# Performance work log

Hardware: AMD Instinct MI355X
Metric: run time of the kernel (lower is better)

The kernel has to match this reference:

```python
import jax, jax.numpy as jnp
import numpy as np

B, S, H, L = 4, 1024, 1024, 4
NH, NKV, HD = 16, 8, 64
F, V, W = 3072, 32000, 12
THETA = 1000000.0
EPS = 1e-6
NEG = -1e9


def _rms(x, w):
    return (x * jax.lax.rsqrt(jnp.mean(jnp.square(x), axis=-1, keepdims=True) + EPS)) * w


def _rotate_half(x):
    x1, x2 = jnp.split(x, 2, axis=-1)
    return jnp.concatenate([-x2, x1], axis=-1)


def setup_inputs() -> dict:
    key = jax.random.key(0)
    ks = jax.random.split(key, 16)
    s = 0.02
    return {
        'input_ids': jax.random.randint(ks[0], (B, S), 0, V),
        'attention_mask': jnp.ones((B, S), dtype=jnp.int32),
        'embed': jax.random.normal(ks[1], (V, H), jnp.float32) * s,
        'wq': jax.random.normal(ks[2], (L, H, NH * HD), jnp.float32) * s,
        'wk': jax.random.normal(ks[3], (L, H, NKV * HD), jnp.float32) * s,
        'wv': jax.random.normal(ks[4], (L, H, NKV * HD), jnp.float32) * s,
        'wo': jax.random.normal(ks[5], (L, NH * HD, H), jnp.float32) * s,
        'q_norm_w': jnp.ones((L, HD), jnp.float32),
        'k_norm_w': jnp.ones((L, HD), jnp.float32),
        'ln1': jnp.ones((L, H), jnp.float32),
        'ln2': jnp.ones((L, H), jnp.float32),
        'w_gate': jax.random.normal(ks[6], (L, H, F), jnp.float32) * s,
        'w_up': jax.random.normal(ks[7], (L, H, F), jnp.float32) * s,
        'w_down': jax.random.normal(ks[8], (L, F, H), jnp.float32) * s,
        'final_norm': jnp.ones((H,), jnp.float32),
    }


def _forward(embed, wq, wk, wv, wo, q_norm_w, k_norm_w, ln1, ln2,
             w_gate, w_up, w_down, final_norm, input_ids, attention_mask):
    h = embed[input_ids]                                   # [B,S,H]
    # rotary embeddings (Qwen3 style, theta=1e6)
    pos = jnp.arange(S, dtype=jnp.float32)
    inv_freq = 1.0 / (THETA ** (jnp.arange(0, HD, 2, dtype=jnp.float32) / HD))
    freqs = pos[:, None] * inv_freq[None, :]               # [S, HD/2]
    emb = jnp.concatenate([freqs, freqs], axis=-1)         # [S, HD]
    cos = jnp.cos(emb)[None, :, None, :]
    sin = jnp.sin(emb)[None, :, None, :]
    # masks: full = expanded (non-causal) padding mask; sliding = +/-W band
    pad = (1.0 - attention_mask.astype(jnp.float32))[:, None, None, :] * NEG
    idx = jnp.arange(S)
    band = jnp.abs(idx[:, None] - idx[None, :]) <= W       # [S,S]
    full_mask = jnp.broadcast_to(pad, (B, 1, S, S))
    slide_mask = jnp.where(band[None, None], full_mask, NEG)
    scale = 1.0 / np.sqrt(HD).astype(np.float32)
    for l in range(L):
        mask = full_mask if l % 2 == 0 else slide_mask     # attention_type dispatch
        x = _rms(h, ln1[l])
        q = _rms((x @ wq[l]).reshape(B, S, NH, HD), q_norm_w[l])
        k = _rms((x @ wk[l]).reshape(B, S, NKV, HD), k_norm_w[l])
        v = (x @ wv[l]).reshape(B, S, NKV, HD)
        q = q * cos + _rotate_half(q) * sin
        k = k * cos + _rotate_half(k) * sin
        rep = NH // NKV                                    # GQA expand
        k = jnp.repeat(k, rep, axis=2)
        v = jnp.repeat(v, rep, axis=2)
        scores = jnp.einsum('bqhd,bkhd->bhqk', q, k) * scale + mask
        p = jax.nn.softmax(scores, axis=-1)
        attn = jnp.einsum('bhqk,bkhd->bqhd', p, v).reshape(B, S, NH * HD)
        h = h + attn @ wo[l]
        x = _rms(h, ln2[l])
        h = h + (jax.nn.silu(x @ w_gate[l]) * (x @ w_up[l])) @ w_down[l]
    return _rms(h, final_norm)


def reference(input_ids, attention_mask, embed, wq, wk, wv, wo, q_norm_w, k_norm_w,
              ln1, ln2, w_gate, w_up, w_down, final_norm):
    return _forward(embed, wq, wk, wv, wo, q_norm_w, k_norm_w, ln1, ln2,
                    w_gate, w_up, w_down, final_norm, input_ids, attention_mask)
```

## Files before the change

kernel.cpp:

```cpp
#include <hip/hip_runtime.h>
#include <math.h>

#define BB 4
#define SS 1024
#define HH 1024
#define LL 4
#define NHH 16
#define NKV 8
#define HD 64
#define FF 3072
#define WW 12
#define NEG_INF (-1e9f)

#define OQ  0
#define OK_ 1048576
#define OV  1572864
#define OO  2097152
#define OG  3145728
#define OU  6291456
#define OD  9437184

typedef __attribute__((ext_vector_type(8))) short bf16x8;
typedef __attribute__((ext_vector_type(4))) float f32x4;
typedef __attribute__((ext_vector_type(16))) float f32x16;
typedef __attribute__((ext_vector_type(8))) unsigned short u16x8;

__device__ __forceinline__ unsigned short f2bf(float f) {
    union { float f; unsigned int u; } v; v.f = f;
    unsigned int r = (v.u + 0x7fffu + ((v.u >> 16) & 1u)) >> 16;
    return (unsigned short)r;
}
__device__ __forceinline__ float bf2f(unsigned short u) {
    union { unsigned int u; float f; } v; v.u = ((unsigned int)u) << 16;
    return v.f;
}
__device__ __forceinline__ unsigned int pkbf(float lo, float hi) {
    return (unsigned int)f2bf(lo) | ((unsigned int)f2bf(hi) << 16);
}
__device__ __forceinline__ void gll16(const void* g, void* l) {
    __builtin_amdgcn_global_load_lds((const __attribute__((address_space(1))) void*)g,
                                     (__attribute__((address_space(3))) void*)l, 16, 0, 0);
}

__global__ __launch_bounds__(256) void k_embed(const int* __restrict__ ids,
                                               const float* __restrict__ embed,
                                               float* __restrict__ h) {
    int row = blockIdx.x, tid = threadIdx.x;
    int id = ids[row];
    ((float4*)(h + (size_t)row * HH))[tid] = ((const float4*)(embed + (size_t)id * HH))[tid];
}

__global__ __launch_bounds__(256) void k_rms_bf16(const float* __restrict__ in,
                                                  const float* __restrict__ w,
                                                  unsigned short* __restrict__ out) {
    __shared__ float red[4];
    int row = blockIdx.x, tid = threadIdx.x;
    float4 v = ((const float4*)(in + (size_t)row * HH))[tid];
    float ss = v.x * v.x + v.y * v.y + v.z * v.z + v.w * v.w;
#pragma unroll
    for (int off = 1; off < 64; off <<= 1) ss += __shfl_xor(ss, off);
    if ((tid & 63) == 0) red[tid >> 6] = ss;
    __syncthreads();
    float tot = red[0] + red[1] + red[2] + red[3];
    float scale = rsqrtf(tot * (1.0f / HH) + 1e-6f);
    float4 wv = ((const float4*)w)[tid];
    ushort4 o;
    o.x = f2bf(v.x * scale * wv.x); o.y = f2bf(v.y * scale * wv.y);
    o.z = f2bf(v.z * scale * wv.z); o.w = f2bf(v.w * scale * wv.w);
    *(ushort4*)&out[(size_t)row * HH + tid * 4] = o;
}

template <int NP, int BF16OUT>
__global__ __launch_bounds__(256) void k_rms_add(float* __restrict__ h,
                                                 const float* __restrict__ p0,
                                                 const float* __restrict__ p1,
                                                 const float* __restrict__ p2,
                                                 const float* __restrict__ w,
                                                 void* __restrict__ outx) {
    __shared__ float red[4];
    int row = blockIdx.x, tid = threadIdx.x;
    size_t base = (size_t)row * HH;
    float4 v = ((const float4*)(h + base))[tid];
    float4 a = ((const float4*)(p0 + base))[tid];
    v.x += a.x; v.y += a.y; v.z += a.z; v.w += a.w;
    if (NP > 1) {
        float4 b = ((const float4*)(p1 + base))[tid];
        v.x += b.x; v.y += b.y; v.z += b.z; v.w += b.w;
    }
    if (NP > 2) {
        float4 c = ((const float4*)(p2 + base))[tid];
        v.x += c.x; v.y += c.y; v.z += c.z; v.w += c.w;
    }
    ((float4*)(h + base))[tid] = v;
    float ss = v.x * v.x + v.y * v.y + v.z * v.z + v.w * v.w;
#pragma unroll
    for (int off = 1; off < 64; off <<= 1) ss += __shfl_xor(ss, off);
    if ((tid & 63) == 0) red[tid >> 6] = ss;
    __syncthreads();
    float tot = red[0] + red[1] + red[2] + red[3];
    float scale = rsqrtf(tot * (1.0f / HH) + 1e-6f);
    float4 wv = ((const float4*)w)[tid];
    float rx = v.x * scale * wv.x, ry = v.y * scale * wv.y;
    float rz = v.z * scale * wv.z, rw = v.w * scale * wv.w;
    if (BF16OUT) {
        ushort4 o;
        o.x = f2bf(rx); o.y = f2bf(ry); o.z = f2bf(rz); o.w = f2bf(rw);
        *(ushort4*)&((unsigned short*)outx)[base + tid * 4] = o;
    } else {
        float4 o; o.x = rx; o.y = ry; o.z = rz; o.w = rw;
        ((float4*)((float*)outx + base))[tid] = o;
    }
}

__global__ __launch_bounds__(256) void k_cast_all(const float* __restrict__ wq,
                                                  const float* __restrict__ wk,
                                                  const float* __restrict__ wv,
                                                  const float* __restrict__ wo,
                                                  const float* __restrict__ wg,
                                                  const float* __restrict__ wu,
                                                  const float* __restrict__ wd,
                                                  unsigned short* __restrict__ wbf) {
    __shared__ float t[64][65];
    int tI = blockIdx.x;
    const float* W; unsigned short* Wt; int N, K, local;
    if (tI < 256)       { W = wq; Wt = wbf + OQ;  N = 1024; K = 1024; local = tI; }
    else if (tI < 384)  { W = wk; Wt = wbf + OK_; N = 512;  K = 1024; local = tI - 256; }
    else if (tI < 512)  { W = wv; Wt = wbf + OV;  N = 512;  K = 1024; local = tI - 384; }
    else if (tI < 768)  { W = wo; Wt = wbf + OO;  N = 1024; K = 1024; local = tI - 512; }
    else if (tI < 1536) { W = wg; Wt = wbf + OG;  N = 3072; K = 1024; local = tI - 768; }
    else if (tI < 2304) { W = wu; Wt = wbf + OU;  N = 3072; K = 1024; local = tI - 1536; }
    else                { W = wd; Wt = wbf + OD;  N = 1024; K = 3072; local = tI - 2304; }
    int tn = N >> 6;
    int n0 = (local % tn) * 64, k0 = (local / tn) * 64;
    int tid = threadIdx.x;
    int r = tid >> 4;
    int c4 = (tid & 15) * 4;
#pragma unroll
    for (int e = 0; e < 4; ++e) {
        int kk = r + e * 16;
        float4 vv = *(const float4*)&W[(size_t)(k0 + kk) * N + n0 + c4];
        t[c4 + 0][kk] = vv.x;
        t[c4 + 1][kk] = vv.y;
        t[c4 + 2][kk] = vv.z;
        t[c4 + 3][kk] = vv.w;
    }
    __syncthreads();
#pragma unroll
    for (int e = 0; e < 4; ++e) {
        int nn = r + e * 16;
        ushort4 o;
        o.x = f2bf(t[nn][c4 + 0]);
        o.y = f2bf(t[nn][c4 + 1]);
        o.z = f2bf(t[nn][c4 + 2]);
        o.w = f2bf(t[nn][c4 + 3]);
        *(ushort4*)&Wt[(size_t)(n0 + nn) * K + k0 + c4] = o;
    }
}

template <int EPI>
__device__ __forceinline__ void mgemm_core(const unsigned short* __restrict__ A,
                                           const unsigned short* __restrict__ Bt,
                                           void* __restrict__ Cv,
                                           int N, int K, int lda, int ldb,
                                           int bm, int bn) {
    __shared__ unsigned short As[128 * 32];
    __shared__ unsigned short Bs[128 * 32];
    int tid = threadIdx.x;
    int w = tid >> 6, l = tid & 63;
    int wr = (w >> 1) * 64, wc = (w & 1) * 64;

    f32x4 acc[4][4] = {};

    for (int k0 = 0; k0 < K; k0 += 32) {
        __syncthreads();
#pragma unroll
        for (int i = 0; i < 2; ++i) {
            int cb = i * 256 + w * 64;
            int c = cb + l;
            const unsigned short* ga = A + (size_t)(bm + (c >> 2)) * lda + k0 + (c & 3) * 8;
            const unsigned short* gb = Bt + (size_t)(bn + (c >> 2)) * ldb + k0 + (c & 3) * 8;
            gll16(ga, As + cb * 8);
            gll16(gb, Bs + cb * 8);
        }
        __syncthreads();

        bf16x8 af[4], bfr[4];
#pragma unroll
        for (int i = 0; i < 4; ++i) {
            int m = wr + i * 16 + (l & 15);
            af[i] = *(const bf16x8*)&As[m * 32 + (l >> 4) * 8];
            int n = wc + i * 16 + (l & 15);
            bfr[i] = *(const bf16x8*)&Bs[n * 32 + (l >> 4) * 8];
        }
#pragma unroll
        for (int i = 0; i < 4; ++i)
#pragma unroll
            for (int j = 0; j < 4; ++j)
                acc[i][j] = __builtin_amdgcn_mfma_f32_16x16x32_bf16(af[i], bfr[j], acc[i][j], 0, 0, 0);
    }

#pragma unroll
    for (int i = 0; i < 4; ++i) {
        int rbase = bm + wr + i * 16 + (l >> 4) * 4;
#pragma unroll
        for (int j = 0; j < 4; ++j) {
            int col = bn + wc + j * 16 + (l & 15);
#pragma unroll
            for (int r = 0; r < 4; ++r) {
                size_t off = (size_t)(rbase + r) * N + col;
                if (EPI == 0) ((float*)Cv)[off] = acc[i][j][r];
                else if (EPI == 1) ((float*)Cv)[off] += acc[i][j][r];
                else ((unsigned short*)Cv)[off] = f2bf(acc[i][j][r]);
            }
        }
    }
}

template <int PARTS>
__global__ __launch_bounds__(256) void k_mgemm_splitk(const unsigned short* __restrict__ A,
                                                      const unsigned short* __restrict__ Bt,
                                                      float* __restrict__ p0,
                                                      float* __restrict__ p1,
                                                      float* __restrict__ p2,
                                                      int N, int Ktot) {
    int part = blockIdx.z;
    int Kp = Ktot / PARTS;
    float* C = (part == 0) ? p0 : (part == 1 ? p1 : p2);
    mgemm_core<0>(A + part * Kp, Bt + part * Kp, C, N, Kp, Ktot, Ktot,
                  blockIdx.y * 128, blockIdx.x * 128);
}

__global__ __launch_bounds__(256) void k_mgemm_qkv(const unsigned short* __restrict__ A,
                                                   const unsigned short* __restrict__ wqt,
                                                   const unsigned short* __restrict__ wkt,
                                                   const unsigned short* __restrict__ wvt,
                                                   float* __restrict__ q,
                                                   float* __restrict__ k,
                                                   unsigned short* __restrict__ v) {
    int nt = blockIdx.x;
    if (nt < 8)       mgemm_core<0>(A, wqt, q, 1024, 1024, 1024, 1024, blockIdx.y * 128, nt * 128);
    else if (nt < 12) mgemm_core<0>(A, wkt, k, 512, 1024, 1024, 1024, blockIdx.y * 128, (nt - 8) * 128);
    else              mgemm_core<2>(A, wvt, v, 512, 1024, 1024, 1024, blockIdx.y * 128, (nt - 12) * 128);
}

__global__ __launch_bounds__(256) void k_mgemm_gu(const unsigned short* __restrict__ A,
                                                  const unsigned short* __restrict__ wgt,
                                                  const unsigned short* __restrict__ wut,
                                                  unsigned short* __restrict__ g,
                                                  unsigned short* __restrict__ u) {
    int nt = blockIdx.x;
    const unsigned short* Bt = (nt < 24) ? wgt : wut;
    unsigned short* C = (nt < 24) ? g : u;
    int bn = (nt < 24 ? nt : nt - 24) * 128;
    mgemm_core<2>(A, Bt, C, 3072, 1024, 1024, 1024, blockIdx.y * 128, bn);
}

__global__ __launch_bounds__(256) void k_qknorm_rope(const float* __restrict__ qk,
                                                     unsigned short* __restrict__ out,
                                                     const float* __restrict__ nw,
                                                     int nheads) {
    int tid = threadIdx.x;
    int w = tid >> 6, lane = tid & 63;
    int gid = blockIdx.x * 4 + w;
    int row = gid / nheads;
    int pos = row & (SS - 1);
    size_t base = (size_t)gid * HD;
    float xv = qk[base + lane];
    float ss = xv * xv;
#pragma unroll
    for (int off = 1; off < 64; off <<= 1) ss += __shfl_xor(ss, off);
    float scale = rsqrtf(ss * (1.0f / HD) + 1e-6f);
    float xn = xv * scale * nw[lane];
    int j = lane & 31;
    float inv_freq = powf(1.0e6f, -(float)j * (1.0f / 32.0f));
    float f = (float)pos * inv_freq;
    float c = cosf(f), s = sinf(f);
    float partner = __shfl_xor(xn, 32);
    float rot = (lane < 32) ? -partner : partner;
    out[base + lane] = f2bf(xn * c + rot * s);
}

__global__ __launch_bounds__(256) void k_mattn(const unsigned short* __restrict__ q,
                                               const unsigned short* __restrict__ k,
                                               const unsigned short* __restrict__ v,
                                               const int* __restrict__ amask,
                                               unsigned short* __restrict__ out,
                                               int sliding) {
    __shared__ __align__(16) char smem[18432];
    unsigned short* Klds = (unsigned short*)smem;
    unsigned int*   VtU  = (unsigned int*)(smem + 8192);
    float* mlds          = (float*)(smem + 17152);
    unsigned short* Olds = (unsigned short*)smem;

    const int b = blockIdx.z, head = blockIdx.y, q0 = blockIdx.x * 128;
    const int kvh = head >> 1;
    const int tid = threadIdx.x, w = tid >> 6, lane = tid & 63;
    const int h = lane >> 5, ln31 = lane & 31;
    const int qg = q0 + w * 32 + ln31;
    const float sscale = 0.125f;

    bf16x8 qf[4];
    const unsigned short* qrow = q + (size_t)(b * SS + qg) * 1024 + head * 64;
#pragma unroll
    for (int c = 0; c < 4; ++c) qf[c] = *(const bf16x8*)(qrow + c * 16 + h * 8);

    f32x16 O0 = {}, O1 = {};
    float m = -3.4e38f, l_sum = 0.0f;

    int t_lo = 0, t_hi = (SS >> 6) - 1;
    if (sliding) {
        int lo = q0 - WW; if (lo < 0) lo = 0;
        int hi = q0 + 127 + WW; if (hi > SS - 1) hi = SS - 1;
        t_lo = lo >> 6; t_hi = hi >> 6;
    }

    const int vd = tid & 63, vw = tid >> 6;

    for (int t = t_lo; t <= t_hi; ++t) {
        int kv0 = t << 6;
        __syncthreads();
        if (tid < 64) mlds[tid] = amask[b * SS + kv0 + tid] ? 0.0f : NEG_INF;
#pragma unroll
        for (int i = 0; i < 2; ++i) {
            int slot = i * 256 + w * 64 + lane;
            int row = slot >> 3, u = slot & 7;
            int ug = u ^ (row & 7);
            const unsigned short* src = k + (size_t)(b * SS + kv0 + row) * 512 + kvh * 64 + ug * 8;
            gll16(src, Klds + (size_t)slot * 8);
        }
        {
            const unsigned short* vsrc = v + (size_t)(b * SS + kv0 + vw * 16) * 512 + kvh * 64 + vd;
            unsigned short tmp[16];
#pragma unroll
            for (int kk = 0; kk < 16; ++kk) tmp[kk] = vsrc[(size_t)kk * 512];
#pragma unroll
            for (int j = 0; j < 8; ++j)
                VtU[vd * 35 + vw * 8 + j] =
                    (unsigned int)tmp[2 * j] | ((unsigned int)tmp[2 * j + 1] << 16);
        }
        __syncthreads();

        f32x16 a0 = {}, a1 = {};
#pragma unroll
        for (int c = 0; c < 4; ++c) {
            int u = (2 * c + h) ^ (ln31 & 7);
            bf16x8 k0 = *(const bf16x8*)&Klds[ln31 * 64 + u * 8];
            bf16x8 k1 = *(const bf16x8*)&Klds[(32 + ln31) * 64 + u * 8];
            a0 = __builtin_amdgcn_mfma_f32_32x32x16_bf16(k0, qf[c], a0, 0, 0, 0);
            a1 = __builtin_amdgcn_mfma_f32_32x32x16_bf16(k1, qf[c], a1, 0, 0, 0);
        }

        float tmax = -3.4e38f;
#pragma unroll
        for (int r = 0; r < 16; ++r) {
            int kl = (r & 3) + 8 * (r >> 2) + 4 * h;
            float mv0 = mlds[kl], mv1 = mlds[32 + kl];
            if (sliding) {
                int d0 = qg - (kv0 + kl); if (d0 < 0) d0 = -d0;
                int d1 = qg - (kv0 + 32 + kl); if (d1 < 0) d1 = -d1;
                if (d0 > WW) mv0 = NEG_INF;
                if (d1 > WW) mv1 = NEG_INF;
            }
            a0[r] = a0[r] * sscale + mv0;
            a1[r] = a1[r] * sscale + mv1;
            tmax = fmaxf(tmax, fmaxf(a0[r], a1[r]));
        }
        tmax = fmaxf(tmax, __shfl_xor(tmax, 32));
        float nm = fmaxf(m, tmax);
        float corr = __expf(m - nm);
        float tsum = 0.0f;
#pragma unroll
        for (int r = 0; r < 16; ++r) {
            a0[r] = __expf(a0[r] - nm);
            a1[r] = __expf(a1[r] - nm);
            tsum += a0[r] + a1[r];
        }
        tsum += __shfl_xor(tsum, 32);
        l_sum = l_sum * corr + tsum;
#pragma unroll
        for (int r = 0; r < 16; ++r) { O0[r] *= corr; O1[r] *= corr; }
        m = nm;

#pragma unroll
        for (int s = 0; s < 2; ++s) {
#pragma unroll
            for (int c2 = 0; c2 < 2; ++c2) {
                float p0v = s ? a1[8 * c2 + 0] : a0[8 * c2 + 0];
                float p1v = s ? a1[8 * c2 + 1] : a0[8 * c2 + 1];
                float p2v = s ? a1[8 * c2 + 2] : a0[8 * c2 + 2];
                float p3v = s ? a1[8 * c2 + 3] : a0[8 * c2 + 3];
                float p4v = s ? a1[8 * c2 + 4] : a0[8 * c2 + 4];
                float p5v = s ? a1[8 * c2 + 5] : a0[8 * c2 + 5];
                float p6v = s ? a1[8 * c2 + 6] : a0[8 * c2 + 6];
                float p7v = s ? a1[8 * c2 + 7] : a0[8 * c2 + 7];
                unsigned int A0 = pkbf(p0v, p1v);
                unsigned int A1 = pkbf(p2v, p3v);
                unsigned int A2 = pkbf(p4v, p5v);
                unsigned int A3 = pkbf(p6v, p7v);
                unsigned int pA0 = (unsigned int)__shfl_xor((int)A0, 32);
                unsigned int pA1 = (unsigned int)__shfl_xor((int)A1, 32);
                unsigned int pA2 = (unsigned int)__shfl_xor((int)A2, 32);
                unsigned int pA3 = (unsigned int)__shfl_xor((int)A3, 32);
                union { unsigned int u[4]; bf16x8 v; } pf;
                pf.u[0] = h ? pA2 : A0;
                pf.u[1] = h ? pA3 : A1;
                pf.u[2] = h ? A2 : pA0;
                pf.u[3] = h ? A3 : pA1;
#pragma unroll
                for (int dt = 0; dt < 2; ++dt) {
                    int base = (dt * 32 + ln31) * 35 + s * 16 + c2 * 8 + h * 4;
                    union { unsigned int u[4]; bf16x8 v; } vf;
                    vf.u[0] = VtU[base + 0];
                    vf.u[1] = VtU[base + 1];
                    vf.u[2] = VtU[base + 2];
                    vf.u[3] = VtU[base + 3];
                    if (dt == 0) O0 = __builtin_amdgcn_mfma_f32_32x32x16_bf16(vf.v, pf.v, O0, 0, 0, 0);
                    else         O1 = __builtin_amdgcn_mfma_f32_32x32x16_bf16(vf.v, pf.v, O1, 0, 0, 0);
                }
            }
        }
    }

    __syncthreads();
    float rl = 1.0f / l_sum;
    unsigned short* myO = Olds + w * 2240;
#pragma unroll
    for (int dt = 0; dt < 2; ++dt)
#pragma unroll
        for (int r = 0; r < 16; ++r) {
            int d = dt * 32 + (r & 3) + 8 * (r >> 2) + 4 * h;
            float val = (dt ? O1[r] : O0[r]) * rl;
            myO[ln31 * 70 + d] = f2bf(val);
        }
    int qr = lane >> 1, half = lane & 1;
    const unsigned int* osrc = (const unsigned int*)Olds + (size_t)w * 1120 + qr * 35 + half * 16;
    unsigned int vals[16];
#pragma unroll
    for (int j = 0; j < 16; ++j) vals[j] = osrc[j];
    unsigned short* dst = out + (size_t)(b * SS + q0 + w * 32 + qr) * 1024 + head * 64 + half * 32;
#pragma unroll
    for (int j = 0; j < 4; ++j)
        ((uint4*)dst)[j] = make_uint4(vals[4 * j], vals[4 * j + 1], vals[4 * j + 2], vals[4 * j + 3]);
}

__global__ __launch_bounds__(256) void k_silu_bf16(unsigned short* __restrict__ g,
                                                   const unsigned short* __restrict__ u) {
    int i = blockIdx.x * 256 + threadIdx.x;
    u16x8 gv = ((const u16x8*)g)[i];
    u16x8 uv = ((const u16x8*)u)[i];
    u16x8 o;
#pragma unroll
    for (int j = 0; j < 8; ++j) {
        float gf = bf2f(gv[j]), uf = bf2f(uv[j]);
        o[j] = f2bf(gf / (1.0f + __expf(-gf)) * uf);
    }
    ((u16x8*)g)[i] = o;
}

extern "C" void kernel_launch(void* const* d_in, const int* in_sizes, int n_in,
                              void* d_out, int out_size, void* d_ws, size_t ws_size,
                              hipStream_t stream) {
    const int* input_ids = (const int*)d_in[0];
    const int* amask     = (const int*)d_in[1];
    const float* embed   = (const float*)d_in[2];
    const float* wq      = (const float*)d_in[3];
    const float* wk      = (const float*)d_in[4];
    const float* wv      = (const float*)d_in[5];
    const float* wo      = (const float*)d_in[6];
    const float* qnw     = (const float*)d_in[7];
    const float* knw     = (const float*)d_in[8];
    const float* ln1     = (const float*)d_in[9];
    const float* ln2     = (const float*)d_in[10];
    const float* wg      = (const float*)d_in[11];
    const float* wu      = (const float*)d_in[12];
    const float* wd      = (const float*)d_in[13];
    const float* fnorm   = (const float*)d_in[14];
    float* out = (float*)d_out;

    const int ROWS = BB * SS;
    float* h  = (float*)d_ws;
    float* qb = h + (size_t)ROWS * HH;
    float* kb = qb + (size_t)ROWS * HH;
    unsigned short* xb  = (unsigned short*)(kb + (size_t)ROWS * (NKV * HD));
    unsigned short* qbf = xb + (size_t)ROWS * HH;
    unsigned short* kbf = qbf + (size_t)ROWS * HH;
    unsigned short* vbf = kbf + (size_t)ROWS * (NKV * HD);
    unsigned short* gbf = vbf + (size_t)ROWS * (NKV * HD);
    unsigned short* ubf = gbf + (size_t)ROWS * FF;
    unsigned short* wbf = ubf + (size_t)ROWS * FF;

    k_embed<<<ROWS, 256, 0, stream>>>(input_ids, embed, h);
    k_rms_bf16<<<ROWS, 256, 0, stream>>>(h, ln1, xb);

    for (int l = 0; l < LL; ++l) {
        const float* wq_l = wq + (size_t)l * HH * (NHH * HD);
        const float* wk_l = wk + (size_t)l * HH * (NKV * HD);
        const float* wv_l = wv + (size_t)l * HH * (NKV * HD);
        const float* wo_l = wo + (size_t)l * (NHH * HD) * HH;
        const float* wg_l = wg + (size_t)l * HH * FF;
        const float* wu_l = wu + (size_t)l * HH * FF;
        const float* wd_l = wd + (size_t)l * FF * HH;

        k_cast_all<<<3072, 256, 0, stream>>>(wq_l, wk_l, wv_l, wo_l, wg_l, wu_l, wd_l, wbf);

        k_mgemm_qkv<<<dim3(16, 32), 256, 0, stream>>>(xb, wbf + OQ, wbf + OK_, wbf + OV,
                                                      qb, kb, vbf);

        k_qknorm_rope<<<ROWS * NHH / 4, 256, 0, stream>>>(qb, qbf, qnw + l * HD, NHH);
        k_qknorm_rope<<<ROWS * NKV / 4, 256, 0, stream>>>(kb, kbf, knw + l * HD, NKV);

        k_mattn<<<dim3(SS / 128, NHH, BB), 256, 0, stream>>>(qbf, kbf, vbf, amask, xb, l & 1);

        k_mgemm_splitk<2><<<dim3(8, 32, 2), 256, 0, stream>>>(xb, wbf + OO, qb, (float*)gbf,
                                                              nullptr, 1024, 1024);
        k_rms_add<2, 1><<<ROWS, 256, 0, stream>>>(h, qb, (float*)gbf, nullptr,
                                                  ln2 + l * HH, xb);

        k_mgemm_gu<<<dim3(48, 32), 256, 0, stream>>>(xb, wbf + OG, wbf + OU, gbf, ubf);

        k_silu_bf16<<<ROWS * FF / 8 / 256, 256, 0, stream>>>(gbf, ubf);

        k_mgemm_splitk<3><<<dim3(8, 32, 3), 256, 0, stream>>>(gbf, wbf + OD, qb, (float*)ubf,
                                                              (float*)wbf, 1024, 3072);
        if (l < LL - 1) {
            k_rms_add<3, 1><<<ROWS, 256, 0, stream>>>(h, qb, (float*)ubf, (float*)wbf,
                                                      ln1 + (l + 1) * HH, xb);
        } else {
            k_rms_add<3, 0><<<ROWS, 256, 0, stream>>>(h, qb, (float*)ubf, (float*)wbf,
                                                      fnorm, out);
        }
    }
}
```

Baseline: 1.412 ms.

## Double-buffer GEMM LDS tiles and split-K the fused QKV projection

```diff
diff --git a/kernel.cpp b/kernel.cpp
--- a/kernel.cpp
+++ b/kernel.cpp
@@ -163,41 +163,51 @@
                                            void* __restrict__ Cv,
                                            int N, int K, int lda, int ldb,
                                            int bm, int bn) {
-    __shared__ unsigned short As[128 * 32];
-    __shared__ unsigned short Bs[128 * 32];
+    __shared__ unsigned short As[2][128 * 32];
+    __shared__ unsigned short Bs[2][128 * 32];
     int tid = threadIdx.x;
     int w = tid >> 6, l = tid & 63;
     int wr = (w >> 1) * 64, wc = (w & 1) * 64;
 
     f32x4 acc[4][4] = {};
 
-    for (int k0 = 0; k0 < K; k0 += 32) {
-        __syncthreads();
-#pragma unroll
-        for (int i = 0; i < 2; ++i) {
-            int cb = i * 256 + w * 64;
-            int c = cb + l;
-            const unsigned short* ga = A + (size_t)(bm + (c >> 2)) * lda + k0 + (c & 3) * 8;
-            const unsigned short* gb = Bt + (size_t)(bn + (c >> 2)) * ldb + k0 + (c & 3) * 8;
-            gll16(ga, As + cb * 8);
-            gll16(gb, Bs + cb * 8);
-        }
-        __syncthreads();
+#define MG_STAGE(s, k0)                                                               \
+    {                                                                                 \
+        _Pragma("unroll")                                                             \
+        for (int i = 0; i < 2; ++i) {                                                 \
+            int cb = i * 256 + w * 64;                                                \
+            int c = cb + l;                                                           \
+            const unsigned short* ga = A + (size_t)(bm + (c >> 2)) * lda + (k0) + (c & 3) * 8; \
+            const unsigned short* gb = Bt + (size_t)(bn + (c >> 2)) * ldb + (k0) + (c & 3) * 8; \
+            gll16(ga, &As[s][cb * 8]);                                                \
+            gll16(gb, &Bs[s][cb * 8]);                                                \
+        }                                                                             \
+    }
+
+    MG_STAGE(0, 0);
+    __syncthreads();
+
+    int nt = K >> 5;
+    for (int t = 0; t < nt; ++t) {
+        int cur = t & 1;
+        if (t + 1 < nt) MG_STAGE(cur ^ 1, (t + 1) * 32);
 
         bf16x8 af[4], bfr[4];
 #pragma unroll
         for (int i = 0; i < 4; ++i) {
             int m = wr + i * 16 + (l & 15);
-            af[i] = *(const bf16x8*)&As[m * 32 + (l >> 4) * 8];
+            af[i] = *(const bf16x8*)&As[cur][m * 32 + (l >> 4) * 8];
             int n = wc + i * 16 + (l & 15);
-            bfr[i] = *(const bf16x8*)&Bs[n * 32 + (l >> 4) * 8];
+            bfr[i] = *(const bf16x8*)&Bs[cur][n * 32 + (l >> 4) * 8];
         }
 #pragma unroll
         for (int i = 0; i < 4; ++i)
 #pragma unroll
             for (int j = 0; j < 4; ++j)
                 acc[i][j] = __builtin_amdgcn_mfma_f32_16x16x32_bf16(af[i], bfr[j], acc[i][j], 0, 0, 0);
-    }
+        __syncthreads();
+    }
+#undef MG_STAGE
 
 #pragma unroll
     for (int i = 0; i < 4; ++i) {
@@ -222,25 +232,12 @@
                                                       float* __restrict__ p0,
                                                       float* __restrict__ p1,
                                                       float* __restrict__ p2,
-                                                      int N, int Ktot) {
+                                                      int N, int Ktot, int lda) {
     int part = blockIdx.z;
     int Kp = Ktot / PARTS;
     float* C = (part == 0) ? p0 : (part == 1 ? p1 : p2);
-    mgemm_core<0>(A + part * Kp, Bt + part * Kp, C, N, Kp, Ktot, Ktot,
+    mgemm_core<0>(A + part * Kp, Bt + part * Kp, C, N, Kp, lda, Ktot,
                   blockIdx.y * 128, blockIdx.x * 128);
-}
-
-__global__ __launch_bounds__(256) void k_mgemm_qkv(const unsigned short* __restrict__ A,
-                                                   const unsigned short* __restrict__ wqt,
-                                                   const unsigned short* __restrict__ wkt,
-                                                   const unsigned short* __restrict__ wvt,
-                                                   float* __restrict__ q,
-                                                   float* __restrict__ k,
-                                                   unsigned short* __restrict__ v) {
-    int nt = blockIdx.x;
-    if (nt < 8)       mgemm_core<0>(A, wqt, q, 1024, 1024, 1024, 1024, blockIdx.y * 128, nt * 128);
-    else if (nt < 12) mgemm_core<0>(A, wkt, k, 512, 1024, 1024, 1024, blockIdx.y * 128, (nt - 8) * 128);
-    else              mgemm_core<2>(A, wvt, v, 512, 1024, 1024, 1024, blockIdx.y * 128, (nt - 12) * 128);
 }
 
 __global__ __launch_bounds__(256) void k_mgemm_gu(const unsigned short* __restrict__ A,
@@ -255,17 +252,19 @@
     mgemm_core<2>(A, Bt, C, 3072, 1024, 1024, 1024, blockIdx.y * 128, bn);
 }
 
-__global__ __launch_bounds__(256) void k_qknorm_rope(const float* __restrict__ qk,
+__global__ __launch_bounds__(256) void k_qknorm_rope(const float* __restrict__ p0,
+                                                     const float* __restrict__ p1,
                                                      unsigned short* __restrict__ out,
                                                      const float* __restrict__ nw,
-                                                     int nheads) {
+                                                     int nheads, int coloff) {
     int tid = threadIdx.x;
     int w = tid >> 6, lane = tid & 63;
     int gid = blockIdx.x * 4 + w;
     int row = gid / nheads;
+    int head = gid - row * nheads;
     int pos = row & (SS - 1);
-    size_t base = (size_t)gid * HD;
-    float xv = qk[base + lane];
+    size_t src = (size_t)row * 2048 + coloff + head * 64 + lane;
+    float xv = p0[src] + p1[src];
     float ss = xv * xv;
 #pragma unroll
     for (int off = 1; off < 64; off <<= 1) ss += __shfl_xor(ss, off);
@@ -277,7 +276,24 @@
     float c = cosf(f), s = sinf(f);
     float partner = __shfl_xor(xn, 32);
     float rot = (lane < 32) ? -partner : partner;
-    out[base + lane] = f2bf(xn * c + rot * s);
+    out[(size_t)gid * HD + lane] = f2bf(xn * c + rot * s);
+}
+
+__global__ __launch_bounds__(256) void k_vred(const float* __restrict__ p0,
+                                              const float* __restrict__ p1,
+                                              unsigned short* __restrict__ v) {
+    int i = blockIdx.x * 256 + threadIdx.x;
+    int row = i >> 6;
+    int c = (i & 63) * 8;
+    size_t base = (size_t)row * 2048 + 1536 + c;
+    float4 a0 = *(const float4*)&p0[base], a1 = *(const float4*)&p0[base + 4];
+    float4 b0 = *(const float4*)&p1[base], b1 = *(const float4*)&p1[base + 4];
+    u16x8 o;
+    o[0] = f2bf(a0.x + b0.x); o[1] = f2bf(a0.y + b0.y);
+    o[2] = f2bf(a0.z + b0.z); o[3] = f2bf(a0.w + b0.w);
+    o[4] = f2bf(a1.x + b1.x); o[5] = f2bf(a1.y + b1.y);
+    o[6] = f2bf(a1.z + b1.z); o[7] = f2bf(a1.w + b1.w);
+    *(u16x8*)&v[(size_t)row * 512 + c] = o;
 }
 
 __global__ __launch_bounds__(256) void k_mattn(const unsigned short* __restrict__ q,
@@ -478,16 +494,16 @@
     float* out = (float*)d_out;
 
     const int ROWS = BB * SS;
-    float* h  = (float*)d_ws;
-    float* qb = h + (size_t)ROWS * HH;
-    float* kb = qb + (size_t)ROWS * HH;
-    unsigned short* xb  = (unsigned short*)(kb + (size_t)ROWS * (NKV * HD));
+    float* h = (float*)d_ws;
+    unsigned short* xb  = (unsigned short*)(h + (size_t)ROWS * HH);
     unsigned short* qbf = xb + (size_t)ROWS * HH;
     unsigned short* kbf = qbf + (size_t)ROWS * HH;
     unsigned short* vbf = kbf + (size_t)ROWS * (NKV * HD);
     unsigned short* gbf = vbf + (size_t)ROWS * (NKV * HD);
     unsigned short* ubf = gbf + (size_t)ROWS * FF;
     unsigned short* wbf = ubf + (size_t)ROWS * FF;
+    float* P0 = (float*)(wbf + 12582912);
+    float* P1 = P0 + (size_t)ROWS * 2048;
 
     k_embed<<<ROWS, 256, 0, stream>>>(input_ids, embed, h);
     k_rms_bf16<<<ROWS, 256, 0, stream>>>(h, ln1, xb);
@@ -503,30 +519,30 @@
 
         k_cast_all<<<3072, 256, 0, stream>>>(wq_l, wk_l, wv_l, wo_l, wg_l, wu_l, wd_l, wbf);
 
-        k_mgemm_qkv<<<dim3(16, 32), 256, 0, stream>>>(xb, wbf + OQ, wbf + OK_, wbf + OV,
-                                                      qb, kb, vbf);
-
-        k_qknorm_rope<<<ROWS * NHH / 4, 256, 0, stream>>>(qb, qbf, qnw + l * HD, NHH);
-        k_qknorm_rope<<<ROWS * NKV / 4, 256, 0, stream>>>(kb, kbf, knw + l * HD, NKV);
+        k_mgemm_splitk<2><<<dim3(16, 32, 2), 256, 0, stream>>>(xb, wbf + OQ, P0, P1,
+                                                               nullptr, 2048, 1024, 1024);
+
+        k_qknorm_rope<<<ROWS * NHH / 4, 256, 0, stream>>>(P0, P1, qbf, qnw + l * HD, NHH, 0);
+        k_qknorm_rope<<<ROWS * NKV / 4, 256, 0, stream>>>(P0, P1, kbf, knw + l * HD, NKV, 1024);
+        k_vred<<<ROWS * 512 / 8 / 256, 256, 0, stream>>>(P0, P1, vbf);
 
         k_mattn<<<dim3(SS / 128, NHH, BB), 256, 0, stream>>>(qbf, kbf, vbf, amask, xb, l & 1);
 
-        k_mgemm_splitk<2><<<dim3(8, 32, 2), 256, 0, stream>>>(xb, wbf + OO, qb, (float*)gbf,
-                                                              nullptr, 1024, 1024);
-        k_rms_add<2, 1><<<ROWS, 256, 0, stream>>>(h, qb, (float*)gbf, nullptr,
-                                                  ln2 + l * HH, xb);
+        k_mgemm_splitk<2><<<dim3(8, 32, 2), 256, 0, stream>>>(xb, wbf + OO, P0, P1,
+                                                              nullptr, 1024, 1024, 1024);
+        k_rms_add<2, 1><<<ROWS, 256, 0, stream>>>(h, P0, P1, nullptr, ln2 + l * HH, xb);
 
         k_mgemm_gu<<<dim3(48, 32), 256, 0, stream>>>(xb, wbf + OG, wbf + OU, gbf, ubf);
 
         k_silu_bf16<<<ROWS * FF / 8 / 256, 256, 0, stream>>>(gbf, ubf);
 
-        k_mgemm_splitk<3><<<dim3(8, 32, 3), 256, 0, stream>>>(gbf, wbf + OD, qb, (float*)ubf,
-                                                              (float*)wbf, 1024, 3072);
+        k_mgemm_splitk<3><<<dim3(8, 32, 3), 256, 0, stream>>>(gbf, wbf + OD, P0, P1,
+                                                              (float*)wbf, 1024, 3072, 3072);
         if (l < LL - 1) {
-            k_rms_add<3, 1><<<ROWS, 256, 0, stream>>>(h, qb, (float*)ubf, (float*)wbf,
+            k_rms_add<3, 1><<<ROWS, 256, 0, stream>>>(h, P0, P1, (float*)wbf,
                                                       ln1 + (l + 1) * HH, xb);
         } else {
-            k_rms_add<3, 0><<<ROWS, 256, 0, stream>>>(h, qb, (float*)ubf, (float*)wbf,
+            k_rms_add<3, 0><<<ROWS, 256, 0, stream>>>(h, P0, P1, (float*)wbf,
                                                       fnorm, out);
         }
     }
```

Result: no change. 1.433 ms (+1.5%).
